# Optimization experiments

Measured on AMD Instinct MI355X. Metric: run time of the kernel, lower is better.

## Reference

```python
import jax, jax.numpy as jnp
import numpy as np


def _conv1x1(x_flat, W, b):
    # x_flat: [B, Cin, N], W: [Cout, Cin], b: [Cout]
    return jnp.einsum('oc,bcn->bon', W, x_flat) + b[None, :, None]


def setup_inputs() -> dict:
    key = jax.random.key(0)
    ks = jax.random.split(key, 7)
    B, C, H, W = 8, 64, 64, 64
    Ch = C // 2
    s_in = 1.0 / np.sqrt(C)
    x = jax.random.normal(ks[0], (B, C, H, W), dtype=jnp.float32)
    Wb = jax.random.uniform(ks[1], (Ch, C), jnp.float32, -s_in, s_in)
    bb = jax.random.uniform(ks[2], (Ch,), jnp.float32, -s_in, s_in)
    Wc = jax.random.uniform(ks[3], (Ch, C), jnp.float32, -s_in, s_in)
    bc = jax.random.uniform(ks[4], (Ch,), jnp.float32, -s_in, s_in)
    Wd = jax.random.uniform(ks[5], (C, C), jnp.float32, -s_in, s_in)
    bd = jax.random.uniform(ks[6], (C,), jnp.float32, -s_in, s_in)
    return {'x': x, 'Wb': Wb, 'bb': bb, 'Wc': Wc, 'bc': bc, 'Wd': Wd, 'bd': bd}


def reference(x, Wb, bb, Wc, bc, Wd, bd):
    B, C, H, Wd_ = x.shape
    N = H * Wd_
    x_flat = x.reshape(B, C, N)
    feat_b = _conv1x1(x_flat, Wb, bb)            # [B, C/2, N]
    feat_c = _conv1x1(x_flat, Wc, bc)            # [B, C/2, N]
    # scores[b,n,m] = sum_c feat_b[b,c,n] * feat_c[b,c,m]
    scores = jnp.einsum('bcn,bcm->bnm', feat_b, feat_c)
    attn = jax.nn.softmax(scores, axis=-1)       # [B, N, N]
    feat_d = _conv1x1(x_flat, Wd, bd)            # [B, C, N]
    # feat_e[b,c,m] = sum_n feat_d[b,c,n] * attn[b,m,n]  (bmm with attn^T)
    feat_e = jnp.einsum('bcn,bmn->bcm', feat_d, attn)
    return feat_e.reshape(B, C, H, Wd_) + x
```

## Files before the change

### kernel.cpp

```cpp
#include <hip/hip_runtime.h>

#define N_TOK 4096
#define L2E 1.44269504088896340736f
#define SH2 (14.0f * L2E)

typedef short bf16x8 __attribute__((ext_vector_type(8)));
typedef float f32x4 __attribute__((ext_vector_type(4)));
typedef float f32x16 __attribute__((ext_vector_type(16)));
typedef unsigned int u32x4 __attribute__((ext_vector_type(4)));
typedef unsigned short u16x4 __attribute__((ext_vector_type(4)));

static __device__ __forceinline__ unsigned short f2bf(float f) {
    unsigned int u = __builtin_bit_cast(unsigned int, f);
    u += 0x7FFFu + ((u >> 16) & 1u);
    return (unsigned short)(u >> 16);
}

__global__ __launch_bounds__(256) void proj_kernel(
    const float* __restrict__ x,
    const float* __restrict__ Wb, const float* __restrict__ bb,
    const float* __restrict__ Wc, const float* __restrict__ bc,
    const float* __restrict__ Wd, const float* __restrict__ bd,
    unsigned short* __restrict__ Qg, unsigned short* __restrict__ Kg,
    unsigned short* __restrict__ VgT)
{
    const int b   = blockIdx.y;
    const int n0  = blockIdx.x * 64;
    const int tid = threadIdx.x;

    __shared__ unsigned short Wl[128 * 72];
    __shared__ unsigned short xT[64 * 72];
    __shared__ float bl[128];

    #pragma unroll
    for (int i = 0; i < 32; ++i) {
        int e = i * 256 + tid;
        int row = e >> 6, c = e & 63;
        float v;
        if (row < 32)      v = Wb[row * 64 + c];
        else if (row < 64) v = Wc[(row - 32) * 64 + c];
        else               v = Wd[(row - 64) * 64 + c];
        Wl[row * 72 + c] = f2bf(v);
    }
    if (tid < 128) {
        float v;
        if (tid < 32)      v = bb[tid];
        else if (tid < 64) v = bc[tid - 32];
        else               v = bd[tid - 64];
        bl[tid] = v;
    }
    #pragma unroll
    for (int i = 0; i < 16; ++i) {
        int e = i * 256 + tid;
        int c = e >> 6, nn = e & 63;
        xT[nn * 72 + c] = f2bf(x[((b * 64 + c) << 12) + n0 + nn]);
    }
    __syncthreads();

    const int w = tid >> 6, l = tid & 63;
    const int lrow = l & 15, lk = (l >> 4) * 8;

    const f32x4 vzero = {0.f, 0.f, 0.f, 0.f};
    f32x4 acc[2][4];
    #pragma unroll
    for (int rt = 0; rt < 2; ++rt)
        #pragma unroll
        for (int ct = 0; ct < 4; ++ct)
            acc[rt][ct] = vzero;

    #pragma unroll
    for (int kb = 0; kb < 2; ++kb) {
        bf16x8 af[2];
        #pragma unroll
        for (int rt = 0; rt < 2; ++rt)
            af[rt] = *(const bf16x8*)&Wl[(w * 32 + rt * 16 + lrow) * 72 + kb * 32 + lk];
        #pragma unroll
        for (int ct = 0; ct < 4; ++ct) {
            bf16x8 bfr = *(const bf16x8*)&xT[(ct * 16 + lrow) * 72 + kb * 32 + lk];
            #pragma unroll
            for (int rt = 0; rt < 2; ++rt)
                acc[rt][ct] = __builtin_amdgcn_mfma_f32_16x16x32_bf16(af[rt], bfr, acc[rt][ct], 0, 0, 0);
        }
    }

    #pragma unroll
    for (int rt = 0; rt < 2; ++rt) {
        const int row0 = w * 32 + rt * 16 + ((l >> 4) << 2);
        #pragma unroll
        for (int ct = 0; ct < 4; ++ct) {
            const int n = n0 + ct * 16 + lrow;
            if (row0 < 64) {
                u16x4 pk;
                #pragma unroll
                for (int r = 0; r < 4; ++r)
                    pk[r] = f2bf(acc[rt][ct][r] + bl[row0 + r]);
                unsigned short* dst = (row0 < 32)
                    ? Qg + (size_t)(b * N_TOK + n) * 32 + row0
                    : Kg + (size_t)(b * N_TOK + n) * 32 + (row0 - 32);
                *(u16x4*)dst = pk;
            } else {
                #pragma unroll
                for (int r = 0; r < 4; ++r)
                    VgT[((size_t)(b * 64 + row0 - 64 + r) << 12) + n] =
                        f2bf(acc[rt][ct][r] + bl[row0 + r]);
            }
        }
    }
}

template <int NHALF>
__global__ __launch_bounds__(256) void attn_kernel(
    const unsigned short* __restrict__ Qg,
    const unsigned short* __restrict__ Kg,
    const unsigned short* __restrict__ VgT,
    const float* __restrict__ x,
    float* __restrict__ outp,
    float* __restrict__ Opart,
    float* __restrict__ Ppart)
{
    const int nwg = 256 * NHALF;
    int i = blockIdx.x;
    int wg = (i & 7) * (nwg >> 3) + (i >> 3);
    const int b    = wg / (32 * NHALF);
    const int rem  = wg % (32 * NHALF);
    const int half = (NHALF == 2) ? (rem >> 5) : 0;
    const int qblk = (NHALF == 2) ? (rem & 31) : rem;
    const int q0   = qblk * 128;
    const int jbase = half * (N_TOK / NHALF);
    const int NT    = (N_TOK / NHALF) / 64;

    const int tid = threadIdx.x;
    const int w  = tid >> 6, l = tid & 63;
    const int lc = l & 31, hi = l >> 5;

    __shared__ unsigned short Kl[2][64 * 36];
    __shared__ unsigned short Vt[2][64 * 68];
    __shared__ float den[4][32];

    bf16x8 qf[2];
    #pragma unroll
    for (int kb = 0; kb < 2; ++kb)
        qf[kb] = *(const bf16x8*)&Qg[(size_t)(b * N_TOK + q0 + w * 32 + lc) * 32 + kb * 16 + hi * 8];

    const int kj = tid >> 2, kseg = (tid & 3) * 8;
    const int vc = tid >> 2, vj   = (tid & 3) * 16;
    const size_t kbase = (size_t)(b * N_TOK + jbase + kj) * 32 + kseg;
    const size_t vbase = ((size_t)(b * 64 + vc) << 12) + jbase + vj;

    u32x4 kreg, vreg0, vreg1;

    kreg  = *(const u32x4*)&Kg[kbase];
    vreg0 = *(const u32x4*)&VgT[vbase];
    vreg1 = *(const u32x4*)&VgT[vbase + 8];
    *(u32x4*)&Kl[0][kj * 36 + kseg]   = kreg;
    *(u32x4*)&Vt[0][vc * 68 + vj]     = vreg0;
    *(u32x4*)&Vt[0][vc * 68 + vj + 8] = vreg1;
    if (NT > 1) {
        kreg  = *(const u32x4*)&Kg[kbase + 64 * 32];
        vreg0 = *(const u32x4*)&VgT[vbase + 64];
        vreg1 = *(const u32x4*)&VgT[vbase + 64 + 8];
    }
    __syncthreads();

    const f32x16 z16 = {0.f,0.f,0.f,0.f,0.f,0.f,0.f,0.f,0.f,0.f,0.f,0.f,0.f,0.f,0.f,0.f};
    f32x16 o[2] = {z16, z16};
    float psum = 0.f;

    for (int t = 0; t < NT; ++t) {
        const int cur = t & 1;

        f32x16 s[2];
        #pragma unroll
        for (int jt = 0; jt < 2; ++jt) {
            bf16x8 kf0 = *(const bf16x8*)&Kl[cur][(jt * 32 + lc) * 36 + hi * 8];
            bf16x8 kf1 = *(const bf16x8*)&Kl[cur][(jt * 32 + lc) * 36 + 16 + hi * 8];
            s[jt] = __builtin_amdgcn_mfma_f32_32x32x16_bf16(kf0, qf[0], z16, 0, 0, 0);
            s[jt] = __builtin_amdgcn_mfma_f32_32x32x16_bf16(kf1, qf[1], s[jt], 0, 0, 0);
        }

        unsigned paw[4][4];
        #pragma unroll
        for (int jt = 0; jt < 2; ++jt) {
            float pp[16];
            #pragma unroll
            for (int r = 0; r < 16; ++r) {
                float pv = __builtin_amdgcn_exp2f(s[jt][r] * L2E - SH2);
                psum += pv;
                pp[r] = pv;
            }
            #pragma unroll
            for (int kb2 = 0; kb2 < 2; ++kb2) {
                const int e = kb2 * 8;
                unsigned A, B, C, D;
                asm("v_cvt_pk_bf16_f32 %0, %1, %2" : "=v"(A) : "v"(pp[e + 0]), "v"(pp[e + 1]));
                asm("v_cvt_pk_bf16_f32 %0, %1, %2" : "=v"(B) : "v"(pp[e + 2]), "v"(pp[e + 3]));
                asm("v_cvt_pk_bf16_f32 %0, %1, %2" : "=v"(C) : "v"(pp[e + 4]), "v"(pp[e + 5]));
                asm("v_cvt_pk_bf16_f32 %0, %1, %2" : "=v"(D) : "v"(pp[e + 6]), "v"(pp[e + 7]));
                asm("v_permlane32_swap_b32 %0, %1" : "+v"(A), "+v"(C));
                asm("v_permlane32_swap_b32 %0, %1" : "+v"(B), "+v"(D));
                paw[jt * 2 + kb2][0] = A; paw[jt * 2 + kb2][1] = B;
                paw[jt * 2 + kb2][2] = C; paw[jt * 2 + kb2][3] = D;
            }
        }

        #pragma unroll
        for (int kb = 0; kb < 4; ++kb) {
            u32x4 pw = {paw[kb][0], paw[kb][1], paw[kb][2], paw[kb][3]};
            bf16x8 pa = __builtin_bit_cast(bf16x8, pw);
            #pragma unroll
            for (int cb = 0; cb < 2; ++cb) {
                bf16x8 vf = *(const bf16x8*)&Vt[cur][(cb * 32 + lc) * 68 + kb * 16 + hi * 8];
                o[cb] = __builtin_amdgcn_mfma_f32_32x32x16_bf16(pa, vf, o[cb], 0, 0, 0);
            }
        }

        if (t + 1 < NT) {
            const int alt = cur ^ 1;
            *(u32x4*)&Kl[alt][kj * 36 + kseg]   = kreg;
            *(u32x4*)&Vt[alt][vc * 68 + vj]     = vreg0;
            *(u32x4*)&Vt[alt][vc * 68 + vj + 8] = vreg1;
            if (t + 2 < NT) {
                const int j2 = (t + 2) * 64;
                kreg  = *(const u32x4*)&Kg[kbase + (size_t)j2 * 32];
                vreg0 = *(const u32x4*)&VgT[vbase + j2];
                vreg1 = *(const u32x4*)&VgT[vbase + j2 + 8];
            }
        }
        __syncthreads();
    }

    float tot = psum + __shfl_xor(psum, 32, 64);

    if (NHALF == 1) {
        if (hi == 0) den[w][lc] = __builtin_amdgcn_rcpf(tot);
        __syncthreads();
        #pragma unroll
        for (int cb = 0; cb < 2; ++cb) {
            const int c = cb * 32 + lc;
            #pragma unroll
            for (int g2 = 0; g2 < 4; ++g2) {
                const int qb = q0 + w * 32 + g2 * 8 + hi * 4;
                f32x4 rinv = *(const f32x4*)&den[w][g2 * 8 + hi * 4];
                const size_t idx = (size_t)(b * 64 + c) * N_TOK + qb;
                f32x4 xv = *(const f32x4*)&x[idx];
                f32x4 ov;
                #pragma unroll
                for (int r = 0; r < 4; ++r)
                    ov[r] = o[cb][g2 * 4 + r] * rinv[r] + xv[r];
                *(f32x4*)&outp[idx] = ov;
            }
        }
    } else {
        #pragma unroll
        for (int cb = 0; cb < 2; ++cb) {
            const size_t cidx = (size_t)((half * 8 + b) * 64 + cb * 32 + lc) * N_TOK;
            #pragma unroll
            for (int g2 = 0; g2 < 4; ++g2) {
                const int qb = q0 + w * 32 + g2 * 8 + hi * 4;
                f32x4 ov = {o[cb][g2 * 4 + 0], o[cb][g2 * 4 + 1],
                            o[cb][g2 * 4 + 2], o[cb][g2 * 4 + 3]};
                *(f32x4*)&Opart[cidx + qb] = ov;
            }
        }
        if (hi == 0)
            Ppart[(size_t)(half * 8 + b) * N_TOK + q0 + w * 32 + lc] = tot;
    }
}

__global__ __launch_bounds__(256) void combine_kernel(
    const float* __restrict__ Opart, const float* __restrict__ Ppart,
    const float* __restrict__ x, float* __restrict__ outp)
{
    const int i = blockIdx.x * 256 + threadIdx.x;
    const int q  = (i & 1023) << 2;
    const int bc = i >> 10;
    const int b  = bc >> 6;
    const size_t obase = ((size_t)bc << 12) + q;

    f32x4 o0 = *(const f32x4*)&Opart[obase];
    f32x4 o1 = *(const f32x4*)&Opart[((size_t)512 << 12) + obase];
    f32x4 p0 = *(const f32x4*)&Ppart[((size_t)b << 12) + q];
    f32x4 p1 = *(const f32x4*)&Ppart[((size_t)(8 + b) << 12) + q];
    f32x4 xv = *(const f32x4*)&x[obase];
    f32x4 ov;
    #pragma unroll
    for (int r = 0; r < 4; ++r)
        ov[r] = (o0[r] + o1[r]) * __builtin_amdgcn_rcpf(p0[r] + p1[r]) + xv[r];
    *(f32x4*)&outp[obase] = ov;
}

extern "C" void kernel_launch(void* const* d_in, const int* in_sizes, int n_in,
                              void* d_out, int out_size, void* d_ws, size_t ws_size,
                              hipStream_t stream) {
    const float* x  = (const float*)d_in[0];
    const float* Wb = (const float*)d_in[1];
    const float* bb = (const float*)d_in[2];
    const float* Wc = (const float*)d_in[3];
    const float* bc = (const float*)d_in[4];
    const float* Wd = (const float*)d_in[5];
    const float* bd = (const float*)d_in[6];
    float* out = (float*)d_out;

    unsigned short* Qg  = (unsigned short*)d_ws;
    unsigned short* Kg  = Qg + (size_t)8 * N_TOK * 32;
    unsigned short* VgT = Kg + (size_t)8 * N_TOK * 32;
    float* Opart = (float*)((char*)d_ws + (size_t)8 * 1024 * 1024);
    float* Ppart = (float*)((char*)d_ws + (size_t)24 * 1024 * 1024);

    proj_kernel<<<dim3(64, 8), 256, 0, stream>>>(x, Wb, bb, Wc, bc, Wd, bd, Qg, Kg, VgT);

    if (ws_size >= (size_t)25 * 1024 * 1024) {
        attn_kernel<2><<<512, 256, 0, stream>>>(Qg, Kg, VgT, x, out, Opart, Ppart);
        combine_kernel<<<2048, 256, 0, stream>>>(Opart, Ppart, x, out);
    } else {
        attn_kernel<1><<<256, 256, 0, stream>>>(Qg, Kg, VgT, x, out, nullptr, nullptr);
    }
}
```

Measured before the change: 62.35 us.

## Split attention keys four ways, fold log2e into Q, and prioritize MFMA phases

Adds a four-way split over the key dimension (1024 workgroups) with a templated combine kernel, used when the workspace is large enough. The log2(e) factor moves into the Q projection and the fixed softmax shift is dropped, so the exp2 argument needs no multiply-add. The P·V MFMA block now runs after the next tile's LDS stores and global prefetch, and both MFMA phases are wrapped in s_setprio to raise wave priority. The aim is better occupancy and latency hiding. The cost is more partial-output traffic and a larger workspace, plus a risk of exp overflow or bf16 range loss without the shift.

Result: no change. 62.12 us (-0.4%).

```diff
diff --git a/kernel.cpp b/kernel.cpp
--- a/kernel.cpp
+++ b/kernel.cpp
@@ -2,7 +2,6 @@
 
 #define N_TOK 4096
 #define L2E 1.44269504088896340736f
-#define SH2 (14.0f * L2E)
 
 typedef short bf16x8 __attribute__((ext_vector_type(8)));
 typedef float f32x4 __attribute__((ext_vector_type(4)));
@@ -92,8 +91,11 @@
             if (row0 < 64) {
                 u16x4 pk;
                 #pragma unroll
-                for (int r = 0; r < 4; ++r)
-                    pk[r] = f2bf(acc[rt][ct][r] + bl[row0 + r]);
+                for (int r = 0; r < 4; ++r) {
+                    float v = acc[rt][ct][r] + bl[row0 + r];
+                    if (row0 < 32) v *= L2E;
+                    pk[r] = f2bf(v);
+                }
                 unsigned short* dst = (row0 < 32)
                     ? Qg + (size_t)(b * N_TOK + n) * 32 + row0
                     : Kg + (size_t)(b * N_TOK + n) * 32 + (row0 - 32);
@@ -123,8 +125,8 @@
     int wg = (i & 7) * (nwg >> 3) + (i >> 3);
     const int b    = wg / (32 * NHALF);
     const int rem  = wg % (32 * NHALF);
-    const int half = (NHALF == 2) ? (rem >> 5) : 0;
-    const int qblk = (NHALF == 2) ? (rem & 31) : rem;
+    const int half = (NHALF >= 2) ? (rem >> 5) : 0;
+    const int qblk = (NHALF >= 2) ? (rem & 31) : rem;
     const int q0   = qblk * 128;
     const int jbase = half * (N_TOK / NHALF);
     const int NT    = (N_TOK / NHALF) / 64;
@@ -170,6 +172,7 @@
         const int cur = t & 1;
 
         f32x16 s[2];
+        __builtin_amdgcn_s_setprio(1);
         #pragma unroll
         for (int jt = 0; jt < 2; ++jt) {
             bf16x8 kf0 = *(const bf16x8*)&Kl[cur][(jt * 32 + lc) * 36 + hi * 8];
@@ -177,6 +180,7 @@
             s[jt] = __builtin_amdgcn_mfma_f32_32x32x16_bf16(kf0, qf[0], z16, 0, 0, 0);
             s[jt] = __builtin_amdgcn_mfma_f32_32x32x16_bf16(kf1, qf[1], s[jt], 0, 0, 0);
         }
+        __builtin_amdgcn_s_setprio(0);
 
         unsigned paw[4][4];
         #pragma unroll
@@ -184,7 +188,7 @@
             float pp[16];
             #pragma unroll
             for (int r = 0; r < 16; ++r) {
-                float pv = __builtin_amdgcn_exp2f(s[jt][r] * L2E - SH2);
+                float pv = __builtin_amdgcn_exp2f(s[jt][r]);
                 psum += pv;
                 pp[r] = pv;
             }
@@ -203,17 +207,6 @@
             }
         }
 
-        #pragma unroll
-        for (int kb = 0; kb < 4; ++kb) {
-            u32x4 pw = {paw[kb][0], paw[kb][1], paw[kb][2], paw[kb][3]};
-            bf16x8 pa = __builtin_bit_cast(bf16x8, pw);
-            #pragma unroll
-            for (int cb = 0; cb < 2; ++cb) {
-                bf16x8 vf = *(const bf16x8*)&Vt[cur][(cb * 32 + lc) * 68 + kb * 16 + hi * 8];
-                o[cb] = __builtin_amdgcn_mfma_f32_32x32x16_bf16(pa, vf, o[cb], 0, 0, 0);
-            }
-        }
-
         if (t + 1 < NT) {
             const int alt = cur ^ 1;
             *(u32x4*)&Kl[alt][kj * 36 + kseg]   = kreg;
@@ -226,6 +219,19 @@
                 vreg1 = *(const u32x4*)&VgT[vbase + j2 + 8];
             }
         }
+
+        __builtin_amdgcn_s_setprio(1);
+        #pragma unroll
+        for (int kb = 0; kb < 4; ++kb) {
+            u32x4 pw = {paw[kb][0], paw[kb][1], paw[kb][2], paw[kb][3]};
+            bf16x8 pa = __builtin_bit_cast(bf16x8, pw);
+            #pragma unroll
+            for (int cb = 0; cb < 2; ++cb) {
+                bf16x8 vf = *(const bf16x8*)&Vt[cur][(cb * 32 + lc) * 68 + kb * 16 + hi * 8];
+                o[cb] = __builtin_amdgcn_mfma_f32_32x32x16_bf16(pa, vf, o[cb], 0, 0, 0);
+            }
+        }
+        __builtin_amdgcn_s_setprio(0);
         __syncthreads();
     }
 
@@ -267,6 +273,7 @@
     }
 }
 
+template <int NHALF>
 __global__ __launch_bounds__(256) void combine_kernel(
     const float* __restrict__ Opart, const float* __restrict__ Ppart,
     const float* __restrict__ x, float* __restrict__ outp)
@@ -277,15 +284,20 @@
     const int b  = bc >> 6;
     const size_t obase = ((size_t)bc << 12) + q;
 
-    f32x4 o0 = *(const f32x4*)&Opart[obase];
-    f32x4 o1 = *(const f32x4*)&Opart[((size_t)512 << 12) + obase];
-    f32x4 p0 = *(const f32x4*)&Ppart[((size_t)b << 12) + q];
-    f32x4 p1 = *(const f32x4*)&Ppart[((size_t)(8 + b) << 12) + q];
+    f32x4 osum = {0.f, 0.f, 0.f, 0.f};
+    f32x4 psum = {0.f, 0.f, 0.f, 0.f};
+    #pragma unroll
+    for (int h = 0; h < NHALF; ++h) {
+        f32x4 oh = *(const f32x4*)&Opart[((size_t)h << 21) + obase];
+        f32x4 ph = *(const f32x4*)&Ppart[((size_t)(h * 8 + b) << 12) + q];
+        #pragma unroll
+        for (int r = 0; r < 4; ++r) { osum[r] += oh[r]; psum[r] += ph[r]; }
+    }
     f32x4 xv = *(const f32x4*)&x[obase];
     f32x4 ov;
     #pragma unroll
     for (int r = 0; r < 4; ++r)
-        ov[r] = (o0[r] + o1[r]) * __builtin_amdgcn_rcpf(p0[r] + p1[r]) + xv[r];
+        ov[r] = osum[r] * __builtin_amdgcn_rcpf(psum[r]) + xv[r];
     *(f32x4*)&outp[obase] = ov;
 }
 
@@ -305,13 +317,17 @@
     unsigned short* Kg  = Qg + (size_t)8 * N_TOK * 32;
     unsigned short* VgT = Kg + (size_t)8 * N_TOK * 32;
     float* Opart = (float*)((char*)d_ws + (size_t)8 * 1024 * 1024);
-    float* Ppart = (float*)((char*)d_ws + (size_t)24 * 1024 * 1024);
 
     proj_kernel<<<dim3(64, 8), 256, 0, stream>>>(x, Wb, bb, Wc, bc, Wd, bd, Qg, Kg, VgT);
 
-    if (ws_size >= (size_t)25 * 1024 * 1024) {
+    if (ws_size >= (size_t)41 * 1024 * 1024) {
+        float* Ppart = (float*)((char*)d_ws + (size_t)40 * 1024 * 1024);
+        attn_kernel<4><<<1024, 256, 0, stream>>>(Qg, Kg, VgT, x, out, Opart, Ppart);
+        combine_kernel<4><<<2048, 256, 0, stream>>>(Opart, Ppart, x, out);
+    } else if (ws_size >= (size_t)25 * 1024 * 1024) {
+        float* Ppart = (float*)((char*)d_ws + (size_t)24 * 1024 * 1024);
         attn_kernel<2><<<512, 256, 0, stream>>>(Qg, Kg, VgT, x, out, Opart, Ppart);
-        combine_kernel<<<2048, 256, 0, stream>>>(Opart, Ppart, x, out);
+        combine_kernel<2><<<2048, 256, 0, stream>>>(Opart, Ppart, x, out);
     } else {
         attn_kernel<1><<<256, 256, 0, stream>>>(Qg, Kg, VgT, x, out, nullptr, nullptr);
     }
```
